# Optimization experiments

Measured on AMD Instinct MI355X. Metric: run time of the kernel, lower is better.

## Reference

```python
import jax, jax.numpy as jnp
import numpy as np

TAU = 0.1
N, D, NUM_CLASSES = 4096, 512, 100


def setup_inputs() -> dict:
    key = jax.random.key(0)
    k1, k2 = jax.random.split(key)
    features = jax.random.normal(k1, (N, D), dtype=jnp.float32)
    targets = jax.random.randint(k2, (N,), 0, NUM_CLASSES, dtype=jnp.int64)
    return {"features": features, "targets": targets}


def reference(features, targets):
    n = features.shape[0]
    # pairwise cosine similarity (with torch-style zero-norm guard)
    sim_mat = features @ features.T                      # [N, N]
    norms = jnp.linalg.norm(features, axis=1)            # [N]
    norm_mat = norms[:, None] * norms[None, :]           # [N, N]
    norm_mat = jnp.where(norm_mat == 0, 1e-8, norm_mat)
    norm_sim = sim_mat / norm_mat
    # positive-pair mask: same class (includes diagonal)
    mask = (targets[None, :] == targets[:, None]).astype(norm_sim.dtype)  # [N, N]
    exp_mat = jnp.exp(norm_sim / TAU)
    eye = jnp.eye(n, dtype=exp_mat.dtype)
    # triu(.,1) + tril(.,-1) == zero out the diagonal
    actual_sim = exp_mat * (1.0 - eye)
    # per-row sum over negatives (mask == 0)
    neg_sum = (actual_sim * (1.0 - mask)).sum(axis=1, keepdims=True)      # [N, 1]
    normalised = actual_sim / (actual_sim + neg_sum) + eye
    positive_cardinality = mask.sum(axis=1, keepdims=True)                # [N, 1]
    loss_mat = -jnp.log(normalised) / positive_cardinality
    loss_mat = jnp.where(jnp.isnan(loss_mat), 0.0, loss_mat)
    contrastive_loss = (loss_mat * mask).sum() / positive_cardinality.sum()
    return contrastive_loss
```

## Files before the change

### kernel.cpp

```cpp
#include <hip/hip_runtime.h>
#include <hip/hip_bf16.h>
#include <math.h>

#define NROWS 4096
#define DIM   512
#define MAXP  128
#define TAU_INV 10.0f
#define NPAN  32
#define TOT   (NPAN*(NPAN+1)/2)
#define CPX   (TOT/8)

using short8 = __attribute__((ext_vector_type(8))) short;
using f32x4  = __attribute__((ext_vector_type(4))) float;

#define OFF_FNB   0
#define OFF_NEG   4194304
#define OFF_RANK  (OFF_NEG  + 16384)
#define OFF_CARD  (OFF_RANK + 16384)
#define OFF_DONE  (OFF_CARD + 16384)
#define OFF_PN    (OFF_DONE + 256)
#define OFF_PD    (OFF_PN   + 256)
#define OFF_PV    (OFF_PD   + 256)

#define GLOBAL_AS __attribute__((address_space(1)))
#define LDS_AS    __attribute__((address_space(3)))

__device__ __forceinline__ void gload_lds16(const void* g, void* l) {
    __builtin_amdgcn_global_load_lds((const GLOBAL_AS unsigned int*)g,
                                     (LDS_AS unsigned int*)l, 16, 0, 0);
}

__device__ __forceinline__ unsigned short f32_to_bf16_rn(float x) {
    unsigned int u = __float_as_uint(x);
    unsigned int r = u + 0x7FFFu + ((u >> 16) & 1u);
    return (unsigned short)(r >> 16);
}

__global__ void k_prep(const float* __restrict__ feat, const int* __restrict__ tgt,
                       unsigned short* __restrict__ fnb,
                       int* __restrict__ rank, int* __restrict__ card,
                       float* __restrict__ negsum, int* __restrict__ done) {
    int tid = threadIdx.x;
    if (blockIdx.x < 4) ((float4*)negsum)[blockIdx.x * 256 + tid] = make_float4(0.f,0.f,0.f,0.f);
    if (blockIdx.x == 4 && tid < 2) done[tid] = 0;
    int w = tid >> 6, l = tid & 63;
    int row = blockIdx.x * 4 + w;
    int myc = tgt[row];
    int call = 0, clt = 0;
    for (int it = 0; it < 64; it++) {
        int j = it * 64 + l;
        int t = tgt[j];
        call += (t == myc);
        clt  += (t == myc && j < row) ? 1 : 0;
    }
    #pragma unroll
    for (int m = 1; m < 64; m <<= 1) {
        call += __shfl_xor(call, m);
        clt  += __shfl_xor(clt, m);
    }
    if (l == 0) { card[row] = call; rank[row] = clt; }
    const float4* src = (const float4*)(feat + (size_t)row * DIM);
    float4 v0 = src[l * 2];
    float4 v1 = src[l * 2 + 1];
    float ss = v0.x*v0.x + v0.y*v0.y + v0.z*v0.z + v0.w*v0.w
             + v1.x*v1.x + v1.y*v1.y + v1.z*v1.z + v1.w*v1.w;
    #pragma unroll
    for (int m = 1; m < 64; m <<= 1) ss += __shfl_xor(ss, m);
    float rs = rsqrtf(fmaxf(ss, 1e-30f));
    float f[8] = { v0.x*rs, v0.y*rs, v0.z*rs, v0.w*rs,
                   v1.x*rs, v1.y*rs, v1.z*rs, v1.w*rs };
    uint4 o;
    o.x = (unsigned)f32_to_bf16_rn(f[0]) | ((unsigned)f32_to_bf16_rn(f[1]) << 16);
    o.y = (unsigned)f32_to_bf16_rn(f[2]) | ((unsigned)f32_to_bf16_rn(f[3]) << 16);
    o.z = (unsigned)f32_to_bf16_rn(f[4]) | ((unsigned)f32_to_bf16_rn(f[5]) << 16);
    o.w = (unsigned)f32_to_bf16_rn(f[6]) | ((unsigned)f32_to_bf16_rn(f[7]) << 16);
    ((uint4*)fnb)[row * 64 + l] = o;
}

__global__ __launch_bounds__(256, 4)
void k_main(const unsigned short* __restrict__ fnb, const int* __restrict__ tgt,
            const int* __restrict__ rank,
            float* __restrict__ negsum, float* __restrict__ posvals)
{
    __shared__ uint4 As4[1024];
    __shared__ uint4 Bs4[1024];
    __shared__ int clsI[128], clsJ[128];
    __shared__ int rkI[128],  rkJ[128];

    int bid = blockIdx.x;
    int b = (bid & 7) * CPX + (bid >> 3);

    int bi = 0, rem = b;
    while (rem >= NPAN - bi) { rem -= NPAN - bi; bi++; }
    int bj = bi + rem;
    bool diag = (bi == bj);
    int i0 = bi * 128, j0 = bj * 128;

    int tid = threadIdx.x;
    if (tid < 128) { clsI[tid] = tgt[i0 + tid];             rkI[tid] = rank[i0 + tid]; }
    else           { clsJ[tid-128] = tgt[j0 + tid-128];     rkJ[tid-128] = rank[j0 + tid-128]; }

    int wid = tid >> 6, l = tid & 63;
    int wr = wid >> 1, wc = wid & 1;

    f32x4 acc[4][4];
    #pragma unroll
    for (int a = 0; a < 4; a++)
        #pragma unroll
        for (int bq = 0; bq < 4; bq++)
            acc[a][bq] = (f32x4){0.f, 0.f, 0.f, 0.f};

    const uint4* gA = (const uint4*)fnb;
    const uint4* Bbase = diag ? As4 : Bs4;

    for (int kt = 0; kt < 8; kt++) {
        #pragma unroll
        for (int p = 0; p < 4; p++) {
            int id = p * 256 + tid;
            int row = id >> 3, cx = id & 7;
            int c = cx ^ (row & 7);
            gload_lds16(&gA[(i0 + row) * 64 + kt * 8 + c], &As4[id]);
            if (!diag)
                gload_lds16(&gA[(j0 + row) * 64 + kt * 8 + c], &Bs4[id]);
        }
        __syncthreads();
        #pragma unroll
        for (int s = 0; s < 2; s++) {
            short8 af[4], bf[4];
            #pragma unroll
            for (int mi = 0; mi < 4; mi++) {
                int row = wr * 64 + mi * 16 + (l & 15);
                int cx = (s * 4 + (l >> 4)) ^ (row & 7);
                af[mi] = *(const short8*)&As4[row * 8 + cx];
            }
            #pragma unroll
            for (int ni = 0; ni < 4; ni++) {
                int row = wc * 64 + ni * 16 + (l & 15);
                int cx = (s * 4 + (l >> 4)) ^ (row & 7);
                bf[ni] = *(const short8*)&Bbase[row * 8 + cx];
            }
            #pragma unroll
            for (int mi = 0; mi < 4; mi++)
                #pragma unroll
                for (int ni = 0; ni < 4; ni++)
                    acc[mi][ni] = __builtin_amdgcn_mfma_f32_16x16x32_bf16(
                        af[mi], bf[ni], acc[mi][ni], 0, 0, 0);
        }
        __syncthreads();
    }

    int cj[4], gj[4], rj[4];
    #pragma unroll
    for (int ni = 0; ni < 4; ni++) {
        int jl = wc * 64 + ni * 16 + (l & 15);
        cj[ni] = clsJ[jl];
        gj[ni] = j0 + jl;
        rj[ni] = rkJ[jl];
    }
    float ns[4][4];
    float cns[4] = {0.f, 0.f, 0.f, 0.f};
    #pragma unroll
    for (int mi = 0; mi < 4; mi++) {
        #pragma unroll
        for (int r = 0; r < 4; r++) {
            int il = wr * 64 + mi * 16 + ((l >> 4) << 2) + r;
            int ci = clsI[il];
            int ri = rkI[il];
            int gi = i0 + il;
            float nacc = 0.f;
            #pragma unroll
            for (int ni = 0; ni < 4; ni++) {
                float p = acc[mi][ni][r] * TAU_INV;
                float e = __expf(p);
                if (ci != cj[ni]) {
                    nacc += e;
                    cns[ni] += e;
                } else if (gi != gj[ni]) {
                    posvals[(size_t)gi * MAXP + rj[ni]] = p;
                    if (!diag)
                        posvals[(size_t)gj[ni] * MAXP + ri] = p;
                }
            }
            ns[mi][r] = nacc;
        }
    }
    #pragma unroll
    for (int mi = 0; mi < 4; mi++) {
        #pragma unroll
        for (int r = 0; r < 4; r++) {
            float v = ns[mi][r];
            v += __shfl_xor(v, 1);
            v += __shfl_xor(v, 2);
            v += __shfl_xor(v, 4);
            v += __shfl_xor(v, 8);
            if ((l & 15) == 0) {
                int il = wr * 64 + mi * 16 + ((l >> 4) << 2) + r;
                atomicAdd(&negsum[i0 + il], v);
            }
        }
    }
    if (!diag) {
        #pragma unroll
        for (int ni = 0; ni < 4; ni++) {
            float v = cns[ni];
            v += __shfl_xor(v, 16);
            v += __shfl_xor(v, 32);
            if (l < 16) atomicAdd(&negsum[gj[ni]], v);
        }
    }
}

__global__ void k_fin(const float* __restrict__ negsum,
                      const int* __restrict__ rank, const int* __restrict__ card,
                      const float* __restrict__ posvals,
                      float* __restrict__ partialN, float* __restrict__ partialD,
                      int* __restrict__ done, float* __restrict__ out)
{
    __shared__ float redN[4], redD[4];
    __shared__ int lastflag;
    int tid = threadIdx.x, w = tid >> 6, l = tid & 63;
    int base = (blockIdx.x * 4 + w) * 16;
    float Sv[16]; int cv[16], rv[16];
    #pragma unroll
    for (int it = 0; it < 16; it++) {
        int row = base + it;
        Sv[it] = negsum[row];
        cv[it] = card[row];
        rv[it] = rank[row];
    }
    float nacc = 0.f, dacc = 0.f;
    #pragma unroll
    for (int it = 0; it < 16; it++) {
        int row = base + it;
        const float* pv = posvals + (size_t)row * MAXP;
        float p0 = pv[l];
        float p1 = pv[l + 64];
        float S = Sv[it]; int cd = cv[it], rk = rv[it];
        float t0 = __logf(__expf(p0) + S) - p0;
        float t1 = __logf(__expf(p1) + S) - p1;
        float t = ((l < cd && l != rk) ? t0 : 0.f)
                + ((l + 64 < cd && l + 64 != rk) ? t1 : 0.f);
        nacc += t / (float)cd;
        if (l == 0) dacc += (float)cd;
    }
    #pragma unroll
    for (int msk = 1; msk < 64; msk <<= 1) {
        nacc += __shfl_xor(nacc, msk);
        dacc += __shfl_xor(dacc, msk);
    }
    if (l == 0) { redN[w] = nacc; redD[w] = dacc; }
    __syncthreads();
    if (tid == 0) {
        partialN[blockIdx.x] = redN[0] + redN[1] + redN[2] + redN[3];
        partialD[blockIdx.x] = redD[0] + redD[1] + redD[2] + redD[3];
        __threadfence();
        int d = atomicAdd(done, 1);
        lastflag = (d == (int)gridDim.x - 1) ? 1 : 0;
    }
    __syncthreads();
    if (lastflag && tid < 64) {
        __threadfence();
        float n = partialN[tid];
        float dd = partialD[tid];
        #pragma unroll
        for (int msk = 1; msk < 64; msk <<= 1) {
            n  += __shfl_xor(n, msk);
            dd += __shfl_xor(dd, msk);
        }
        if (tid == 0) out[0] = n / dd;
    }
}

extern "C" void kernel_launch(void* const* d_in, const int* in_sizes, int n_in,
                              void* d_out, int out_size, void* d_ws, size_t ws_size,
                              hipStream_t stream) {
    (void)in_sizes; (void)n_in; (void)out_size; (void)ws_size;
    const float* feat = (const float*)d_in[0];
    const int*   tgt  = (const int*)d_in[1];
    float* out = (float*)d_out;
    char* ws = (char*)d_ws;

    unsigned short* fnb = (unsigned short*)(ws + OFF_FNB);
    float* negsum  = (float*)(ws + OFF_NEG);
    int*   rank    = (int*)(ws + OFF_RANK);
    int*   card    = (int*)(ws + OFF_CARD);
    int*   done    = (int*)(ws + OFF_DONE);
    float* pN      = (float*)(ws + OFF_PN);
    float* pD      = (float*)(ws + OFF_PD);
    float* posvals = (float*)(ws + OFF_PV);

    k_prep<<<dim3(1024), dim3(256), 0, stream>>>(feat, tgt, fnb, rank, card,
                                                 negsum, done);
    k_main<<<dim3(TOT), dim3(256), 0, stream>>>(fnb, tgt, rank, negsum, posvals);
    k_fin<<<dim3(64), dim3(256), 0, stream>>>(negsum, rank, card, posvals,
                                              pN, pD, done, out);
}
```

Measured before the change: 94.19 us.

## Double-buffer LDS tiles with async global-to-LDS prefetch in main GEMM loop

Splits the A/B shared-memory tiles into two buffers and issues the global-to-LDS loads for the next K-slice before computing on the current one. Manual vmcnt waits and barriers replace the two __syncthreads per iteration, so load latency can overlap the MFMA work. This doubles LDS use, and launch bounds drop from 4 to 2 waves per SIMD, which may reduce occupancy-based latency hiding. Correctness depends on the hand-counted vmcnt values matching the number of outstanding loads.

```diff
diff --git a/kernel.cpp b/kernel.cpp
--- a/kernel.cpp
+++ b/kernel.cpp
@@ -77,13 +77,13 @@
     ((uint4*)fnb)[row * 64 + l] = o;
 }
 
-__global__ __launch_bounds__(256, 4)
+__global__ __launch_bounds__(256, 2)
 void k_main(const unsigned short* __restrict__ fnb, const int* __restrict__ tgt,
             const int* __restrict__ rank,
             float* __restrict__ negsum, float* __restrict__ posvals)
 {
-    __shared__ uint4 As4[1024];
-    __shared__ uint4 Bs4[1024];
+    __shared__ uint4 As4[2][1024];
+    __shared__ uint4 Bs4[2][1024];
     __shared__ int clsI[128], clsJ[128];
     __shared__ int rkI[128],  rkJ[128];
 
@@ -111,43 +111,65 @@
             acc[a][bq] = (f32x4){0.f, 0.f, 0.f, 0.f};
 
     const uint4* gA = (const uint4*)fnb;
-    const uint4* Bbase = diag ? As4 : Bs4;
-
-    for (int kt = 0; kt < 8; kt++) {
-        #pragma unroll
-        for (int p = 0; p < 4; p++) {
-            int id = p * 256 + tid;
-            int row = id >> 3, cx = id & 7;
-            int c = cx ^ (row & 7);
-            gload_lds16(&gA[(i0 + row) * 64 + kt * 8 + c], &As4[id]);
-            if (!diag)
-                gload_lds16(&gA[(j0 + row) * 64 + kt * 8 + c], &Bs4[id]);
-        }
-        __syncthreads();
-        #pragma unroll
-        for (int s = 0; s < 2; s++) {
-            short8 af[4], bf[4];
-            #pragma unroll
-            for (int mi = 0; mi < 4; mi++) {
-                int row = wr * 64 + mi * 16 + (l & 15);
-                int cx = (s * 4 + (l >> 4)) ^ (row & 7);
-                af[mi] = *(const short8*)&As4[row * 8 + cx];
-            }
-            #pragma unroll
-            for (int ni = 0; ni < 4; ni++) {
-                int row = wc * 64 + ni * 16 + (l & 15);
-                int cx = (s * 4 + (l >> 4)) ^ (row & 7);
-                bf[ni] = *(const short8*)&Bbase[row * 8 + cx];
-            }
-            #pragma unroll
-            for (int mi = 0; mi < 4; mi++)
-                #pragma unroll
-                for (int ni = 0; ni < 4; ni++)
-                    acc[mi][ni] = __builtin_amdgcn_mfma_f32_16x16x32_bf16(
-                        af[mi], bf[ni], acc[mi][ni], 0, 0, 0);
-        }
-        __syncthreads();
-    }
+
+    #define STAGE(buf, kt)                                                        \
+        _Pragma("unroll")                                                         \
+        for (int p = 0; p < 4; p++) {                                             \
+            int id = p * 256 + tid;                                               \
+            int row = id >> 3, cx = id & 7;                                       \
+            int c = cx ^ (row & 7);                                               \
+            gload_lds16(&gA[(i0 + row) * 64 + (kt) * 8 + c], &As4[buf][id]);      \
+            if (!diag)                                                            \
+                gload_lds16(&gA[(j0 + row) * 64 + (kt) * 8 + c], &Bs4[buf][id]);  \
+        }
+
+    #define COMPUTE(buf)                                                          \
+        {                                                                         \
+            const uint4* Ab = As4[buf];                                           \
+            const uint4* Bb = diag ? As4[buf] : Bs4[buf];                         \
+            _Pragma("unroll")                                                     \
+            for (int s = 0; s < 2; s++) {                                         \
+                short8 af[4], bf[4];                                              \
+                _Pragma("unroll")                                                 \
+                for (int mi = 0; mi < 4; mi++) {                                  \
+                    int row = wr * 64 + mi * 16 + (l & 15);                       \
+                    int cx = (s * 4 + (l >> 4)) ^ (row & 7);                      \
+                    af[mi] = *(const short8*)&Ab[row * 8 + cx];                   \
+                }                                                                 \
+                _Pragma("unroll")                                                 \
+                for (int ni = 0; ni < 4; ni++) {                                  \
+                    int row = wc * 64 + ni * 16 + (l & 15);                       \
+                    int cx = (s * 4 + (l >> 4)) ^ (row & 7);                      \
+                    bf[ni] = *(const short8*)&Bb[row * 8 + cx];                   \
+                }                                                                 \
+                _Pragma("unroll")                                                 \
+                for (int mi = 0; mi < 4; mi++)                                    \
+                    _Pragma("unroll")                                             \
+                    for (int ni = 0; ni < 4; ni++)                                \
+                        acc[mi][ni] = __builtin_amdgcn_mfma_f32_16x16x32_bf16(    \
+                            af[mi], bf[ni], acc[mi][ni], 0, 0, 0);                \
+            }                                                                     \
+        }
+
+    STAGE(0, 0);
+    int cur = 0;
+    for (int kt = 0; kt < 7; kt++) {
+        STAGE(cur ^ 1, kt + 1);
+        if (diag) { asm volatile("s_waitcnt vmcnt(4)" ::: "memory"); }
+        else      { asm volatile("s_waitcnt vmcnt(8)" ::: "memory"); }
+        __builtin_amdgcn_sched_barrier(0);
+        __builtin_amdgcn_s_barrier();
+        COMPUTE(cur);
+        __builtin_amdgcn_s_barrier();
+        cur ^= 1;
+    }
+    asm volatile("s_waitcnt vmcnt(0)" ::: "memory");
+    __builtin_amdgcn_sched_barrier(0);
+    __builtin_amdgcn_s_barrier();
+    COMPUTE(cur);
+
+    #undef STAGE
+    #undef COMPUTE
 
     int cj[4], gj[4], rj[4];
     #pragma unroll
```

Result: slower. 103.1 us (+9.5%).
